# Optimization experiments

Hardware: AMD Instinct MI355X
Metric: run time of the kernel (lower is better)

Reference implementation:

```python
import jax, jax.numpy as jnp
import numpy as np

B, N = 512, 256
NC = N // 2          # number of SOC (friction-cone) constraints
MAX_ITER = 100       # matches module max_iter
POWER_ITERS = 20     # power iterations for Lipschitz constant estimate


def setup_inputs() -> dict:
    key = jax.random.key(0)
    k1, k2, k3, k4 = jax.random.split(key, 4)
    P = jax.random.normal(k1, (B, N, N), dtype=jnp.float32)
    q = jax.random.normal(k2, (B, N, 1), dtype=jnp.float32)
    l_n = jax.random.uniform(k3, (B, NC, 1), dtype=jnp.float32)
    mu = jax.random.uniform(k4, (B, NC, 1), dtype=jnp.float32)
    return {"P": P, "q": q, "l_n": l_n, "mu": mu}


def _solve(P, b, r):
    # minimize 0.5 * ||P l||^2 + b^T l   s.t.  ||l[2i:2i+2]|| <= r[i]
    # via FISTA (accelerated projected gradient); projection onto a product
    # of 2-D balls is closed-form, honoring the block-SOC structure.
    H = jnp.einsum('bki,bkj->bij', P, P)  # [B,N,N] = P^T P (PSD)

    # Lipschitz constant of grad = lambda_max(H) via power iteration
    def power_step(v, _):
        w = jnp.einsum('bij,bj->bi', H, v)
        v = w / (jnp.linalg.norm(w, axis=-1, keepdims=True) + 1e-12)
        return v, None

    v0 = jnp.ones((B, N), dtype=P.dtype)
    v, _ = jax.lax.scan(power_step, v0, None, length=POWER_ITERS)
    Hv = jnp.einsum('bij,bj->bi', H, v)
    L = jnp.sum(v * Hv, axis=-1) / jnp.sum(v * v, axis=-1)  # [B] Rayleigh quotient
    step = 1.0 / (1.05 * jnp.maximum(L, 1e-12))             # [B]

    def project(l):
        pairs = l.reshape(B, NC, 2)
        nrm = jnp.linalg.norm(pairs, axis=-1)               # [B,NC]
        scale = jnp.where(nrm > r, r / jnp.maximum(nrm, 1e-30), 1.0)
        return (pairs * scale[..., None]).reshape(B, N)

    def fista_step(carry, _):
        l, y, t = carry
        g = jnp.einsum('bij,bj->bi', H, y) + b
        l_new = project(y - step[:, None] * g)
        t_new = 0.5 * (1.0 + jnp.sqrt(1.0 + 4.0 * t * t))
        y_new = l_new + ((t - 1.0) / t_new) * (l_new - l)
        return (l_new, y_new, t_new), None

    l0 = project(jnp.zeros_like(b))
    (l, _, _), _ = jax.lax.scan(fista_step, (l0, l0, jnp.float32(1.0)),
                                None, length=MAX_ITER)
    return l  # [B,N]


def reference(P, q, l_n, mu):
    b = q[..., 0]            # [B,N]
    r = (mu * l_n)[..., 0]   # [B,NC] nonneg SOC radii (mu*l_n in the original)
    return _solve(P, b, r)
```

## Files before the change

kernel.cpp:

```cpp
#include <hip/hip_runtime.h>
#include <math.h>


namespace {

constexpr int NDIM = 256;
constexpr int NCON = 128;
constexpr int PITERS = 20;
constexpr int FITERS = 100;

typedef short bf16x8 __attribute__((ext_vector_type(8)));
typedef float f32x4  __attribute__((ext_vector_type(4)));

struct Smem {
    unsigned short fragHi[16 * 64 * 8];
    unsigned short fragLo[16 * 64 * 8];
    float Hbuf[8][32 * 36];
    float red[2][8][256];
    float ybuf[8][32];
    float scal[16];
};

__device__ __forceinline__ unsigned short bf16rne(float x) {
    unsigned u = __float_as_uint(x);
    unsigned r = u + 0x7FFFu + ((u >> 16) & 1u);
    return (unsigned short)(r >> 16);
}

__device__ __forceinline__ void mv(const float (&h)[128],
                                   const float* __restrict__ xsrc,
                                   float* __restrict__ redw, int l)
{
    float pw0 = 0.f, pw1 = 0.f, pw2 = 0.f, pw3 = 0.f;
#pragma unroll
    for (int jj = 0; jj < 8; ++jj) {
        float4 x4 = *(const float4*)(xsrc + jj * 4);
        pw0 = fmaf(h[0 * 32 + jj * 4 + 0], x4.x, pw0);
        pw0 = fmaf(h[0 * 32 + jj * 4 + 1], x4.y, pw0);
        pw0 = fmaf(h[0 * 32 + jj * 4 + 2], x4.z, pw0);
        pw0 = fmaf(h[0 * 32 + jj * 4 + 3], x4.w, pw0);
        pw1 = fmaf(h[1 * 32 + jj * 4 + 0], x4.x, pw1);
        pw1 = fmaf(h[1 * 32 + jj * 4 + 1], x4.y, pw1);
        pw1 = fmaf(h[1 * 32 + jj * 4 + 2], x4.z, pw1);
        pw1 = fmaf(h[1 * 32 + jj * 4 + 3], x4.w, pw1);
        pw2 = fmaf(h[2 * 32 + jj * 4 + 0], x4.x, pw2);
        pw2 = fmaf(h[2 * 32 + jj * 4 + 1], x4.y, pw2);
        pw2 = fmaf(h[2 * 32 + jj * 4 + 2], x4.z, pw2);
        pw2 = fmaf(h[2 * 32 + jj * 4 + 3], x4.w, pw2);
        pw3 = fmaf(h[3 * 32 + jj * 4 + 0], x4.x, pw3);
        pw3 = fmaf(h[3 * 32 + jj * 4 + 1], x4.y, pw3);
        pw3 = fmaf(h[3 * 32 + jj * 4 + 2], x4.z, pw3);
        pw3 = fmaf(h[3 * 32 + jj * 4 + 3], x4.w, pw3);
    }
    *(float4*)(redw + 4 * l) = make_float4(pw0, pw1, pw2, pw3);
}

__device__ __forceinline__ float2 gather_pair(const float (*red8)[256], int w, int l)
{
    float s0 = 0.f, s1 = 0.f;
#pragma unroll
    for (int c2 = 0; c2 < 8; ++c2) {
        float2 p = *(const float2*)&red8[c2][32 * w + 2 * l];
        s0 += p.x; s1 += p.y;
    }
    return make_float2(s0, s1);
}

__global__ __launch_bounds__(512, 2)
void qcqp_fista(const float* __restrict__ P, const float* __restrict__ q,
                const float* __restrict__ ln_, const float* __restrict__ mu,
                float* __restrict__ out)
{
    __shared__ Smem sm;
    const int b = blockIdx.x;
    const int t = threadIdx.x;
    const int w = t >> 6;
    const int l = t & 63;

    const float* Pb = P + (size_t)b * (NDIM * NDIM);

    const int col  = t & 255;
    const int half = t >> 8;
    const int tile = col >> 4;

    float pf[16];
    auto load_chunk = [&](int cc) {
#pragma unroll
        for (int g = 0; g < 2; ++g) {
            const int qd = 2 * half + g;
            const float* src = Pb + (cc * 32 + qd * 8) * 256 + col;
#pragma unroll
            for (int j = 0; j < 8; ++j) pf[g * 8 + j] = src[j * 256];
        }
    };

    f32x4 acc[16][2];
#pragma unroll
    for (int i = 0; i < 16; ++i)
#pragma unroll
        for (int j = 0; j < 2; ++j)
#pragma unroll
            for (int e = 0; e < 4; ++e) acc[i][j][e] = 0.0f;

    load_chunk(0);
    for (int c = 0; c < 8; ++c) {
#pragma unroll
        for (int g = 0; g < 2; ++g) {
            const int qd = 2 * half + g;
            unsigned hw[4], lw[4];
#pragma unroll
            for (int jp = 0; jp < 4; ++jp) {
                float f0 = pf[g * 8 + 2 * jp], f1 = pf[g * 8 + 2 * jp + 1];
                unsigned short h0 = bf16rne(f0), h1 = bf16rne(f1);
                float r0 = f0 - __uint_as_float((unsigned)h0 << 16);
                float r1 = f1 - __uint_as_float((unsigned)h1 << 16);
                unsigned short lo0 = bf16rne(r0), lo1 = bf16rne(r1);
                hw[jp] = (unsigned)h0 | ((unsigned)h1 << 16);
                lw[jp] = (unsigned)lo0 | ((unsigned)lo1 << 16);
            }
            const int slot = tile * 64 + ((col & 15) + 16 * qd);
            ((uint4*)sm.fragHi)[slot] = make_uint4(hw[0], hw[1], hw[2], hw[3]);
            ((uint4*)sm.fragLo)[slot] = make_uint4(lw[0], lw[1], lw[2], lw[3]);
        }
        __syncthreads();
        if (c < 7) load_chunk(c + 1);

        const bf16x8* FH = (const bf16x8*)sm.fragHi;
        const bf16x8* FL = (const bf16x8*)sm.fragLo;
        bf16x8 bh0 = FH[(2 * w) * 64 + l];
        bf16x8 bl0 = FL[(2 * w) * 64 + l];
        bf16x8 bh1 = FH[(2 * w + 1) * 64 + l];
        bf16x8 bl1 = FL[(2 * w + 1) * 64 + l];
#pragma unroll
        for (int tr = 0; tr < 16; ++tr) {
            bf16x8 ah = FH[tr * 64 + l];
            bf16x8 al = FL[tr * 64 + l];
            acc[tr][0] = __builtin_amdgcn_mfma_f32_16x16x32_bf16(ah, bh0, acc[tr][0], 0, 0, 0);
            acc[tr][0] = __builtin_amdgcn_mfma_f32_16x16x32_bf16(al, bh0, acc[tr][0], 0, 0, 0);
            acc[tr][0] = __builtin_amdgcn_mfma_f32_16x16x32_bf16(ah, bl0, acc[tr][0], 0, 0, 0);
            acc[tr][1] = __builtin_amdgcn_mfma_f32_16x16x32_bf16(ah, bh1, acc[tr][1], 0, 0, 0);
            acc[tr][1] = __builtin_amdgcn_mfma_f32_16x16x32_bf16(al, bh1, acc[tr][1], 0, 0, 0);
            acc[tr][1] = __builtin_amdgcn_mfma_f32_16x16x32_bf16(ah, bl1, acc[tr][1], 0, 0, 0);
        }
        __syncthreads();
    }

    const int qd4 = (l >> 4) * 4;
    const int c16 = l & 15;
    float* Hw = sm.Hbuf[w];
    float h[128];
#pragma unroll
    for (int rc = 0; rc < 8; ++rc) {
#pragma unroll
        for (int tt = 0; tt < 2; ++tt)
#pragma unroll
            for (int tc = 0; tc < 2; ++tc)
#pragma unroll
                for (int reg = 0; reg < 4; ++reg) {
                    int row_local = 16 * tt + qd4 + reg;
                    Hw[row_local * 36 + 16 * tc + c16] = acc[2 * rc + tt][tc][reg];
                }
        if ((l >> 3) == rc) {
            int l2 = l & 7;
#pragma unroll
            for (int e = 0; e < 4; ++e)
#pragma unroll
                for (int jj = 0; jj < 8; ++jj) {
                    float4 v = *(const float4*)&Hw[(4 * l2 + e) * 36 + 4 * jj];
                    h[e * 32 + jj * 4 + 0] = v.x;
                    h[e * 32 + jj * 4 + 1] = v.y;
                    h[e * 32 + jj * 4 + 2] = v.z;
                    h[e * 32 + jj * 4 + 3] = v.w;
                }
        }
    }

    if (l < 32) sm.ybuf[w][l] = 1.0f;
    int phase = 0;
    for (int it = 0; it < PITERS; ++it, ++phase) {
        mv(h, sm.ybuf[w], sm.red[phase & 1][w], l);
        __syncthreads();
        if (l < 16) {
            float2 s = gather_pair(sm.red[phase & 1], w, l);
            *(float2*)&sm.ybuf[w][2 * l] =
                make_float2(s.x * 0.0009765625f, s.y * 0.0009765625f);
        }
    }

    mv(h, sm.ybuf[w], sm.red[phase & 1][w], l);
    __syncthreads();
    float n1 = 0.f, n2 = 0.f;
    if (l < 16) {
        float2 hv = gather_pair(sm.red[phase & 1], w, l);
        float v0 = sm.ybuf[w][2 * l + 0];
        float v1 = sm.ybuf[w][2 * l + 1];
        n1 = v0 * hv.x + v1 * hv.y;
        n2 = v0 * v0 + v1 * v1;
    }
#pragma unroll
    for (int off = 1; off < 64; off <<= 1) {
        n1 += __shfl_xor(n1, off);
        n2 += __shfl_xor(n2, off);
    }
    if (l == 0) { sm.scal[w] = n1; sm.scal[8 + w] = n2; }
    __syncthreads();
    float num = 0.f, den = 0.f;
#pragma unroll
    for (int ww = 0; ww < 8; ++ww) { num += sm.scal[ww]; den += sm.scal[8 + ww]; }
    float L = num / den;
    const float step = 1.0f / (1.05f * fmaxf(L, 1e-12f));
    ++phase;

    float b0 = 0.f, b1 = 0.f, rr = 0.f;
    if (l < 16) {
        float2 q2 = *(const float2*)(q + b * NDIM + 32 * w + 2 * l);
        b0 = q2.x; b1 = q2.y;
        rr = mu[b * NCON + 16 * w + l] * ln_[b * NCON + 16 * w + l];
    }
    float li0 = 0.f, li1 = 0.f, tcur = 1.0f;
    if (l < 32) sm.ybuf[w][l] = 0.0f;

    for (int it = 0; it < FITERS; ++it, ++phase) {
        mv(h, sm.ybuf[w], sm.red[phase & 1][w], l);
        __syncthreads();
        float tn = 0.5f * (1.0f + sqrtf(1.0f + 4.0f * tcur * tcur));
        float ratio = (tcur - 1.0f) / tn;
        tcur = tn;
        if (l < 16) {
            float2 hy = gather_pair(sm.red[phase & 1], w, l);
            float y0 = sm.ybuf[w][2 * l + 0];
            float y1 = sm.ybuf[w][2 * l + 1];
            float z0 = y0 - step * (hy.x + b0);
            float z1 = y1 - step * (hy.y + b1);
            float nrm = sqrtf(z0 * z0 + z1 * z1);
            float scl = (nrm > rr) ? (rr / fmaxf(nrm, 1e-30f)) : 1.0f;
            float l0 = z0 * scl, l1 = z1 * scl;
            float yn0 = l0 + ratio * (l0 - li0);
            float yn1 = l1 + ratio * (l1 - li1);
            li0 = l0; li1 = l1;
            *(float2*)&sm.ybuf[w][2 * l] = make_float2(yn0, yn1);
        }
    }

    if (l < 16)
        *(float2*)(out + b * NDIM + 32 * w + 2 * l) = make_float2(li0, li1);
}

}

extern "C" void kernel_launch(void* const* d_in, const int* in_sizes, int n_in,
                              void* d_out, int out_size, void* d_ws, size_t ws_size,
                              hipStream_t stream) {
    const float* P   = (const float*)d_in[0];
    const float* q   = (const float*)d_in[1];
    const float* l_n = (const float*)d_in[2];
    const float* mu  = (const float*)d_in[3];
    float* out = (float*)d_out;
    qcqp_fista<<<dim3(512), dim3(512), 0, stream>>>(P, q, l_n, mu, out);
}
```

Baseline: 422.4 us.

## Double block to 1024 threads, halving per-thread H registers and MFMA tiles

Each batch block now uses 16 waves instead of 8. Every wave computes half the rows of the Gram matrix via MFMA and holds 64 instead of 128 H values in registers for the iterative matvecs. The 16 waves split the row dimension, and each pair of half-waves redundantly maintains the same y slice. Shared memory is reduced by aliasing the bf16 fragment buffers with the H staging buffer in a union. The goal is more threads per block and lower register pressure for latency hiding in the 120 serial matvec/sync iterations, at the cost of larger-block barriers and duplicated y updates.

```diff
diff --git a/kernel.cpp b/kernel.cpp
--- a/kernel.cpp
+++ b/kernel.cpp
@@ -13,11 +13,15 @@
 typedef float f32x4  __attribute__((ext_vector_type(4)));
 
 struct Smem {
-    unsigned short fragHi[16 * 64 * 8];
-    unsigned short fragLo[16 * 64 * 8];
-    float Hbuf[8][32 * 36];
-    float red[2][8][256];
-    float ybuf[8][32];
+    union {
+        struct {
+            unsigned short fragHi[16 * 64 * 8];
+            unsigned short fragLo[16 * 64 * 8];
+        };
+        float Hbuf[16][32 * 36];
+    };
+    float red[2][16][128];
+    float ybuf[16][32];
     float scal[16];
 };
 
@@ -27,11 +31,11 @@
     return (unsigned short)(r >> 16);
 }
 
-__device__ __forceinline__ void mv(const float (&h)[128],
+__device__ __forceinline__ void mv(const float (&h)[64],
                                    const float* __restrict__ xsrc,
                                    float* __restrict__ redw, int l)
 {
-    float pw0 = 0.f, pw1 = 0.f, pw2 = 0.f, pw3 = 0.f;
+    float pw0 = 0.f, pw1 = 0.f;
 #pragma unroll
     for (int jj = 0; jj < 8; ++jj) {
         float4 x4 = *(const float4*)(xsrc + jj * 4);
@@ -43,30 +47,22 @@
         pw1 = fmaf(h[1 * 32 + jj * 4 + 1], x4.y, pw1);
         pw1 = fmaf(h[1 * 32 + jj * 4 + 2], x4.z, pw1);
         pw1 = fmaf(h[1 * 32 + jj * 4 + 3], x4.w, pw1);
-        pw2 = fmaf(h[2 * 32 + jj * 4 + 0], x4.x, pw2);
-        pw2 = fmaf(h[2 * 32 + jj * 4 + 1], x4.y, pw2);
-        pw2 = fmaf(h[2 * 32 + jj * 4 + 2], x4.z, pw2);
-        pw2 = fmaf(h[2 * 32 + jj * 4 + 3], x4.w, pw2);
-        pw3 = fmaf(h[3 * 32 + jj * 4 + 0], x4.x, pw3);
-        pw3 = fmaf(h[3 * 32 + jj * 4 + 1], x4.y, pw3);
-        pw3 = fmaf(h[3 * 32 + jj * 4 + 2], x4.z, pw3);
-        pw3 = fmaf(h[3 * 32 + jj * 4 + 3], x4.w, pw3);
-    }
-    *(float4*)(redw + 4 * l) = make_float4(pw0, pw1, pw2, pw3);
-}
-
-__device__ __forceinline__ float2 gather_pair(const float (*red8)[256], int w, int l)
+    }
+    *(float2*)(redw + 2 * l) = make_float2(pw0, pw1);
+}
+
+__device__ __forceinline__ float2 gather_pair(const float (*red8)[128], int base)
 {
     float s0 = 0.f, s1 = 0.f;
 #pragma unroll
     for (int c2 = 0; c2 < 8; ++c2) {
-        float2 p = *(const float2*)&red8[c2][32 * w + 2 * l];
+        float2 p = *(const float2*)&red8[c2][base];
         s0 += p.x; s1 += p.y;
     }
     return make_float2(s0, s1);
 }
 
-__global__ __launch_bounds__(512, 2)
+__global__ __launch_bounds__(1024)
 void qcqp_fista(const float* __restrict__ P, const float* __restrict__ q,
                 const float* __restrict__ ln_, const float* __restrict__ mu,
                 float* __restrict__ out)
@@ -74,29 +70,27 @@
     __shared__ Smem sm;
     const int b = blockIdx.x;
     const int t = threadIdx.x;
-    const int w = t >> 6;
-    const int l = t & 63;
+    const int w  = t >> 6;
+    const int l  = t & 63;
+    const int ws = w & 7;
+    const int rh = w >> 3;
 
     const float* Pb = P + (size_t)b * (NDIM * NDIM);
 
     const int col  = t & 255;
-    const int half = t >> 8;
+    const int qd   = t >> 8;
     const int tile = col >> 4;
 
-    float pf[16];
+    float pf[8];
     auto load_chunk = [&](int cc) {
-#pragma unroll
-        for (int g = 0; g < 2; ++g) {
-            const int qd = 2 * half + g;
-            const float* src = Pb + (cc * 32 + qd * 8) * 256 + col;
-#pragma unroll
-            for (int j = 0; j < 8; ++j) pf[g * 8 + j] = src[j * 256];
-        }
+        const float* src = Pb + (cc * 32 + qd * 8) * 256 + col;
+#pragma unroll
+        for (int j = 0; j < 8; ++j) pf[j] = src[j * 256];
     };
 
-    f32x4 acc[16][2];
-#pragma unroll
-    for (int i = 0; i < 16; ++i)
+    f32x4 acc[8][2];
+#pragma unroll
+    for (int i = 0; i < 8; ++i)
 #pragma unroll
         for (int j = 0; j < 2; ++j)
 #pragma unroll
@@ -104,43 +98,39 @@
 
     load_chunk(0);
     for (int c = 0; c < 8; ++c) {
-#pragma unroll
-        for (int g = 0; g < 2; ++g) {
-            const int qd = 2 * half + g;
-            unsigned hw[4], lw[4];
-#pragma unroll
-            for (int jp = 0; jp < 4; ++jp) {
-                float f0 = pf[g * 8 + 2 * jp], f1 = pf[g * 8 + 2 * jp + 1];
-                unsigned short h0 = bf16rne(f0), h1 = bf16rne(f1);
-                float r0 = f0 - __uint_as_float((unsigned)h0 << 16);
-                float r1 = f1 - __uint_as_float((unsigned)h1 << 16);
-                unsigned short lo0 = bf16rne(r0), lo1 = bf16rne(r1);
-                hw[jp] = (unsigned)h0 | ((unsigned)h1 << 16);
-                lw[jp] = (unsigned)lo0 | ((unsigned)lo1 << 16);
-            }
-            const int slot = tile * 64 + ((col & 15) + 16 * qd);
-            ((uint4*)sm.fragHi)[slot] = make_uint4(hw[0], hw[1], hw[2], hw[3]);
-            ((uint4*)sm.fragLo)[slot] = make_uint4(lw[0], lw[1], lw[2], lw[3]);
-        }
+        unsigned hw[4], lw[4];
+#pragma unroll
+        for (int jp = 0; jp < 4; ++jp) {
+            float f0 = pf[2 * jp], f1 = pf[2 * jp + 1];
+            unsigned short h0 = bf16rne(f0), h1 = bf16rne(f1);
+            float r0 = f0 - __uint_as_float((unsigned)h0 << 16);
+            float r1 = f1 - __uint_as_float((unsigned)h1 << 16);
+            unsigned short lo0 = bf16rne(r0), lo1 = bf16rne(r1);
+            hw[jp] = (unsigned)h0 | ((unsigned)h1 << 16);
+            lw[jp] = (unsigned)lo0 | ((unsigned)lo1 << 16);
+        }
+        const int slot = tile * 64 + (col & 15) + 16 * qd;
+        ((uint4*)sm.fragHi)[slot] = make_uint4(hw[0], hw[1], hw[2], hw[3]);
+        ((uint4*)sm.fragLo)[slot] = make_uint4(lw[0], lw[1], lw[2], lw[3]);
         __syncthreads();
         if (c < 7) load_chunk(c + 1);
 
         const bf16x8* FH = (const bf16x8*)sm.fragHi;
         const bf16x8* FL = (const bf16x8*)sm.fragLo;
-        bf16x8 bh0 = FH[(2 * w) * 64 + l];
-        bf16x8 bl0 = FL[(2 * w) * 64 + l];
-        bf16x8 bh1 = FH[(2 * w + 1) * 64 + l];
-        bf16x8 bl1 = FL[(2 * w + 1) * 64 + l];
-#pragma unroll
-        for (int tr = 0; tr < 16; ++tr) {
-            bf16x8 ah = FH[tr * 64 + l];
-            bf16x8 al = FL[tr * 64 + l];
-            acc[tr][0] = __builtin_amdgcn_mfma_f32_16x16x32_bf16(ah, bh0, acc[tr][0], 0, 0, 0);
-            acc[tr][0] = __builtin_amdgcn_mfma_f32_16x16x32_bf16(al, bh0, acc[tr][0], 0, 0, 0);
-            acc[tr][0] = __builtin_amdgcn_mfma_f32_16x16x32_bf16(ah, bl0, acc[tr][0], 0, 0, 0);
-            acc[tr][1] = __builtin_amdgcn_mfma_f32_16x16x32_bf16(ah, bh1, acc[tr][1], 0, 0, 0);
-            acc[tr][1] = __builtin_amdgcn_mfma_f32_16x16x32_bf16(al, bh1, acc[tr][1], 0, 0, 0);
-            acc[tr][1] = __builtin_amdgcn_mfma_f32_16x16x32_bf16(ah, bl1, acc[tr][1], 0, 0, 0);
+        bf16x8 bh0 = FH[(2 * ws) * 64 + l];
+        bf16x8 bl0 = FL[(2 * ws) * 64 + l];
+        bf16x8 bh1 = FH[(2 * ws + 1) * 64 + l];
+        bf16x8 bl1 = FL[(2 * ws + 1) * 64 + l];
+#pragma unroll
+        for (int tt = 0; tt < 8; ++tt) {
+            bf16x8 ah = FH[(8 * rh + tt) * 64 + l];
+            bf16x8 al = FL[(8 * rh + tt) * 64 + l];
+            acc[tt][0] = __builtin_amdgcn_mfma_f32_16x16x32_bf16(ah, bh0, acc[tt][0], 0, 0, 0);
+            acc[tt][0] = __builtin_amdgcn_mfma_f32_16x16x32_bf16(al, bh0, acc[tt][0], 0, 0, 0);
+            acc[tt][0] = __builtin_amdgcn_mfma_f32_16x16x32_bf16(ah, bl0, acc[tt][0], 0, 0, 0);
+            acc[tt][1] = __builtin_amdgcn_mfma_f32_16x16x32_bf16(ah, bh1, acc[tt][1], 0, 0, 0);
+            acc[tt][1] = __builtin_amdgcn_mfma_f32_16x16x32_bf16(al, bh1, acc[tt][1], 0, 0, 0);
+            acc[tt][1] = __builtin_amdgcn_mfma_f32_16x16x32_bf16(ah, bl1, acc[tt][1], 0, 0, 0);
         }
         __syncthreads();
     }
@@ -148,32 +138,34 @@
     const int qd4 = (l >> 4) * 4;
     const int c16 = l & 15;
     float* Hw = sm.Hbuf[w];
-    float h[128];
-#pragma unroll
-    for (int rc = 0; rc < 8; ++rc) {
-#pragma unroll
-        for (int tt = 0; tt < 2; ++tt)
+    float h[64];
+#pragma unroll
+    for (int rc = 0; rc < 4; ++rc) {
+#pragma unroll
+        for (int s = 0; s < 2; ++s)
 #pragma unroll
             for (int tc = 0; tc < 2; ++tc)
 #pragma unroll
-                for (int reg = 0; reg < 4; ++reg) {
-                    int row_local = 16 * tt + qd4 + reg;
-                    Hw[row_local * 36 + 16 * tc + c16] = acc[2 * rc + tt][tc][reg];
+                for (int reg = 0; reg < 4; ++reg)
+                    Hw[(16 * s + qd4 + reg) * 36 + 16 * tc + c16] =
+                        acc[2 * rc + s][tc][reg];
+        if ((l >> 4) == rc) {
+            const int lr = 2 * (l & 15);
+#pragma unroll
+            for (int i = 0; i < 2; ++i)
+#pragma unroll
+                for (int jj = 0; jj < 8; ++jj) {
+                    float4 v = *(const float4*)&Hw[(lr + i) * 36 + 4 * jj];
+                    h[i * 32 + jj * 4 + 0] = v.x;
+                    h[i * 32 + jj * 4 + 1] = v.y;
+                    h[i * 32 + jj * 4 + 2] = v.z;
+                    h[i * 32 + jj * 4 + 3] = v.w;
                 }
-        if ((l >> 3) == rc) {
-            int l2 = l & 7;
-#pragma unroll
-            for (int e = 0; e < 4; ++e)
-#pragma unroll
-                for (int jj = 0; jj < 8; ++jj) {
-                    float4 v = *(const float4*)&Hw[(4 * l2 + e) * 36 + 4 * jj];
-                    h[e * 32 + jj * 4 + 0] = v.x;
-                    h[e * 32 + jj * 4 + 1] = v.y;
-                    h[e * 32 + jj * 4 + 2] = v.z;
-                    h[e * 32 + jj * 4 + 3] = v.w;
-                }
-        }
-    }
+        }
+    }
+
+    const int rhp   = ws >> 2;
+    const int rbase = 32 * (ws & 3);
 
     if (l < 32) sm.ybuf[w][l] = 1.0f;
     int phase = 0;
@@ -181,7 +173,7 @@
         mv(h, sm.ybuf[w], sm.red[phase & 1][w], l);
         __syncthreads();
         if (l < 16) {
-            float2 s = gather_pair(sm.red[phase & 1], w, l);
+            float2 s = gather_pair(&sm.red[phase & 1][8 * rhp], rbase + 2 * l);
             *(float2*)&sm.ybuf[w][2 * l] =
                 make_float2(s.x * 0.0009765625f, s.y * 0.0009765625f);
         }
@@ -191,7 +183,7 @@
     __syncthreads();
     float n1 = 0.f, n2 = 0.f;
     if (l < 16) {
-        float2 hv = gather_pair(sm.red[phase & 1], w, l);
+        float2 hv = gather_pair(&sm.red[phase & 1][8 * rhp], rbase + 2 * l);
         float v0 = sm.ybuf[w][2 * l + 0];
         float v1 = sm.ybuf[w][2 * l + 1];
         n1 = v0 * hv.x + v1 * hv.y;
@@ -202,7 +194,7 @@
         n1 += __shfl_xor(n1, off);
         n2 += __shfl_xor(n2, off);
     }
-    if (l == 0) { sm.scal[w] = n1; sm.scal[8 + w] = n2; }
+    if (l == 0 && rh == 0) { sm.scal[ws] = n1; sm.scal[8 + ws] = n2; }
     __syncthreads();
     float num = 0.f, den = 0.f;
 #pragma unroll
@@ -213,9 +205,9 @@
 
     float b0 = 0.f, b1 = 0.f, rr = 0.f;
     if (l < 16) {
-        float2 q2 = *(const float2*)(q + b * NDIM + 32 * w + 2 * l);
+        float2 q2 = *(const float2*)(q + b * NDIM + 32 * ws + 2 * l);
         b0 = q2.x; b1 = q2.y;
-        rr = mu[b * NCON + 16 * w + l] * ln_[b * NCON + 16 * w + l];
+        rr = mu[b * NCON + 16 * ws + l] * ln_[b * NCON + 16 * ws + l];
     }
     float li0 = 0.f, li1 = 0.f, tcur = 1.0f;
     if (l < 32) sm.ybuf[w][l] = 0.0f;
@@ -227,7 +219,7 @@
         float ratio = (tcur - 1.0f) / tn;
         tcur = tn;
         if (l < 16) {
-            float2 hy = gather_pair(sm.red[phase & 1], w, l);
+            float2 hy = gather_pair(&sm.red[phase & 1][8 * rhp], rbase + 2 * l);
             float y0 = sm.ybuf[w][2 * l + 0];
             float y1 = sm.ybuf[w][2 * l + 1];
             float z0 = y0 - step * (hy.x + b0);
@@ -242,8 +234,8 @@
         }
     }
 
-    if (l < 16)
-        *(float2*)(out + b * NDIM + 32 * w + 2 * l) = make_float2(li0, li1);
+    if (rh == 0 && l < 16)
+        *(float2*)(out + b * NDIM + 32 * ws + 2 * l) = make_float2(li0, li1);
 }
 
 }
@@ -256,5 +248,5 @@
     const float* l_n = (const float*)d_in[2];
     const float* mu  = (const float*)d_in[3];
     float* out = (float*)d_out;
-    qcqp_fista<<<dim3(512), dim3(512), 0, stream>>>(P, q, l_n, mu, out);
-}
+    qcqp_fista<<<dim3(512), dim3(1024), 0, stream>>>(P, q, l_n, mu, out);
+}
```

Result: slower. 454.6 us (+7.6%).
